# Optimization experiments

Hardware: AMD Instinct MI355X
Metric: run time of the kernel (lower is better)

The kernel has to match this reference:

```python
import jax, jax.numpy as jnp
import numpy as np

NUM_HEADS = 12
HEAD_DIM = 128
DIM = NUM_HEADS * HEAD_DIM  # 1536
FRAMES = 8
GRID_H, GRID_W = 15, 26
SPATIAL = GRID_H * GRID_W  # 390
SEQ = FRAMES * SPATIAL      # 3120
EPS = 1e-5


def setup_inputs() -> dict:
    key = jax.random.key(0)
    ks = jax.random.split(key, 12)
    w = lambda k, shape, s=0.02: jax.random.normal(k, shape, dtype=jnp.float32) * s
    return {
        "x": jax.random.normal(ks[0], (1, SEQ, DIM), dtype=jnp.float32),
        "freqs": jax.random.uniform(ks[1], (SEQ, HEAD_DIM // 2), dtype=jnp.float32) * 6.283,
        "Wq": w(ks[2], (DIM, DIM)), "bq": jnp.zeros((DIM,), jnp.float32), "gq": jnp.ones((DIM,), jnp.float32),
        "Wk": w(ks[3], (DIM, DIM)), "bk": jnp.zeros((DIM,), jnp.float32), "gk": jnp.ones((DIM,), jnp.float32),
        "Wv": w(ks[4], (DIM, DIM)), "bv": jnp.zeros((DIM,), jnp.float32),
        "Wo": w(ks[5], (DIM, DIM)), "bo": jnp.zeros((DIM,), jnp.float32),
        "qk_frame_bias": w(ks[6], (FRAMES, DIM), 0.05),
        "v_frame_bias": w(ks[7], (FRAMES, DIM), 0.05),
        "v_spatial_bias": w(ks[8], (SPATIAL, DIM), 0.05),
    }


def _rmsnorm(x, g):
    return x * jax.lax.rsqrt(jnp.mean(x * x, axis=-1, keepdims=True) + EPS) * g


def _rope(x, freqs):
    # x: [b, s, dim] -> per-head interleaved complex rotation (Wan-style)
    b, s, _ = x.shape
    xp = x.reshape(b, s, NUM_HEADS, HEAD_DIM // 2, 2)
    cos = jnp.cos(freqs)[None, :, None, :]  # [1, s, 1, d/2]
    sin = jnp.sin(freqs)[None, :, None, :]
    xr, xi = xp[..., 0], xp[..., 1]
    out = jnp.stack([xr * cos - xi * sin, xr * sin + xi * cos], axis=-1)
    return out.reshape(b, s, DIM)


def _expand_frame(bias):
    # [FRAMES, dim] -> [1, FRAMES*SPATIAL, dim] (each frame vector repeated over spatial tokens)
    return jnp.broadcast_to(bias[:, None, :], (FRAMES, SPATIAL, DIM)).reshape(1, SEQ, DIM)


def _expand_spatial(bias):
    # [SPATIAL, dim] -> [1, FRAMES*SPATIAL, dim] (tiled over frames)
    return jnp.broadcast_to(bias[None, :, :], (FRAMES, SPATIAL, DIM)).reshape(1, SEQ, DIM)


def reference(x, freqs, Wq, bq, gq, Wk, bk, gk, Wv, bv, Wo, bo,
              qk_frame_bias, v_frame_bias, v_spatial_bias):
    q = _rmsnorm(x @ Wq + bq, gq)
    k = _rmsnorm(x @ Wk + bk, gk)
    v = x @ Wv + bv
    q = _rope(q, freqs)
    k = _rope(k, freqs)
    qk_bias = _expand_frame(qk_frame_bias)
    q = q + qk_bias
    k = k + qk_bias
    v = v + _expand_frame(v_frame_bias) + _expand_spatial(v_spatial_bias)
    b, s, _ = x.shape
    qh = q.reshape(b, s, NUM_HEADS, HEAD_DIM)
    kh = k.reshape(b, s, NUM_HEADS, HEAD_DIM)
    vh = v.reshape(b, s, NUM_HEADS, HEAD_DIM)
    scale = 1.0 / np.sqrt(HEAD_DIM)
    scores = jnp.einsum("bqnd,bknd->bnqk", qh, kh) * scale
    attn = jax.nn.softmax(scores, axis=-1)
    out = jnp.einsum("bnqk,bknd->bqnd", attn, vh).reshape(b, s, DIM)
    return out @ Wo + bo
```

## Files before the change

### kernel.cpp

```cpp
#include <hip/hip_runtime.h>
#include <cstdint>

#define SEQ     3120
#define SPAD    3200
#define DIM     1536
#define NQKV    4608
#define HEADS   12
#define HD      128
#define SPATIAL 390
#define EPSV    1e-5f
#define KVBLK   64
#define NTILES  49
#define NEGBIG  (-1e30f)
#define QSCALE  (0.08838834764831845f * 1.4426950408889634f)
#define CROW(r, hi) ((((r) & 3) + 8 * ((r) >> 2)) + 4 * (hi))

typedef unsigned short u16;
typedef short s16x8 __attribute__((ext_vector_type(8)));
typedef float f32x4 __attribute__((ext_vector_type(4)));
typedef float f32x16 __attribute__((ext_vector_type(16)));

__device__ __forceinline__ u16 f2bf(float f) {
  union { float f; unsigned u; } v; v.f = f;
  unsigned r = v.u + 0x7FFFu + ((v.u >> 16) & 1u);
  return (u16)(r >> 16);
}
__device__ __forceinline__ float bf2f(u16 b) {
  union { unsigned u; float f; } v; v.u = ((unsigned)b) << 16;
  return v.f;
}
__device__ __forceinline__ unsigned cvtpk(float lo, float hi) {
  unsigned r;
  asm("v_cvt_pk_bf16_f32 %0, %1, %2" : "=v"(r) : "v"(lo), "v"(hi));
  return r;
}
__device__ __forceinline__ void gload16(const void* g, const void* l) {
  __builtin_amdgcn_global_load_lds(
      (const __attribute__((address_space(1))) unsigned*)g,
      (__attribute__((address_space(3))) unsigned*)(uintptr_t)l,
      16, 0, 0);
}

__global__ __launch_bounds__(256) void k_prep(
    const float* __restrict__ x, const float* __restrict__ bq,
    const float* __restrict__ bk, const float* __restrict__ bv,
    const float* __restrict__ Wq, const float* __restrict__ Wk,
    const float* __restrict__ Wv, const float* __restrict__ Wo,
    u16* __restrict__ xb, float* __restrict__ bcat,
    u16* __restrict__ WtAll, u16* __restrict__ WoT) {
  __shared__ float t[64][65];
  const int bid = blockIdx.x;
  if (bid < 4800) {
    if (bid == 0) {
      for (int j = threadIdx.x; j < NQKV; j += 256)
        bcat[j] = (j < DIM) ? bq[j] : (j < 2 * DIM) ? bk[j - DIM] : bv[j - 2 * DIM];
    }
    const int i = (bid * 256 + threadIdx.x) * 4;
    if (i >= SPAD * DIM) return;
    const int row = i / DIM;
    float4 v = make_float4(0.f, 0.f, 0.f, 0.f);
    if (row < SEQ) v = *(const float4*)(x + i);
    const unsigned lo = (unsigned)f2bf(v.x) | ((unsigned)f2bf(v.y) << 16);
    const unsigned hi = (unsigned)f2bf(v.z) | ((unsigned)f2bf(v.w) << 16);
    *(uint2*)(xb + i) = make_uint2(lo, hi);
  } else {
    const int tb = bid - 4800;
    const int wsel = tb / 576;
    const int rem = tb - wsel * 576;
    const int byi = rem / 24, bxi = rem - (rem / 24) * 24;
    const float* W = (wsel == 0) ? Wq : (wsel == 1) ? Wk : (wsel == 2) ? Wv : Wo;
    const int k0 = bxi * 64, n0 = byi * 64;
    const int c = threadIdx.x & 63, r4 = threadIdx.x >> 6;
#pragma unroll
    for (int rr = 0; rr < 64; rr += 4)
      t[r4 + rr][c] = W[(size_t)(k0 + r4 + rr) * DIM + n0 + c];
    __syncthreads();
    u16* Wt = (wsel < 3) ? (WtAll + (size_t)wsel * DIM * DIM) : WoT;
    const int kp = threadIdx.x & 31;
    const int r8 = threadIdx.x >> 5;
#pragma unroll
    for (int rr = 0; rr < 64; rr += 8) {
      const int n = r8 + rr;
      const unsigned v = (unsigned)f2bf(t[2 * kp][n]) |
                         ((unsigned)f2bf(t[2 * kp + 1][n]) << 16);
      *(unsigned*)&Wt[(size_t)(n0 + n) * DIM + k0 + 2 * kp] = v;
    }
  }
}

template <int OUT_BF16>
__global__ __launch_bounds__(256) void k_gemm(const u16* __restrict__ A,
                                              const u16* __restrict__ Bt,
                                              const float* __restrict__ bias,
                                              void* __restrict__ Cout,
                                              int N, int K, int storeMmax,
                                              int nbx) {
  __shared__ short As[2][8192];
  __shared__ short Bs[2][8192];
  const int nwg = gridDim.x;
  const int q = nwg >> 3, r = nwg & 7;
  const int xcd = blockIdx.x & 7, idx = blockIdx.x >> 3;
  const int swz = (xcd < r ? xcd * (q + 1) : r * (q + 1) + (xcd - r) * q) + idx;
  const int bxi = swz % nbx, byi = swz / nbx;
  const int brow = byi * 128, bcol = bxi * 128;

  const int tid = threadIdx.x;
  const int lane = tid & 63, wv = tid >> 6;
  const int l15 = lane & 15, g = lane >> 4;
  const int wr = wv >> 1, wc = wv & 1;

  const f32x4 z4 = {0.f, 0.f, 0.f, 0.f};
  f32x4 acc[4][4];
#pragma unroll
  for (int m = 0; m < 4; ++m)
#pragma unroll
    for (int n = 0; n < 4; ++n) acc[m][n] = z4;

  const u16* Ap[4];
  const u16* Bp[4];
  const int sch = ((lane & 7) ^ ((lane >> 3) & 7)) * 8;
#pragma unroll
  for (int it = 0; it < 4; ++it) {
    const int row = it * 32 + wv * 8 + (lane >> 3);
    Ap[it] = A + (size_t)(brow + row) * K + sch;
    Bp[it] = Bt + (size_t)(bcol + row) * K + sch;
  }
  auto stage = [&](int T, int B) {
    const int k0 = T * 64;
#pragma unroll
    for (int it = 0; it < 4; ++it) {
      gload16(Ap[it] + k0, &As[B][(it * 32 + wv * 8) * 64]);
      gload16(Bp[it] + k0, &Bs[B][(it * 32 + wv * 8) * 64]);
    }
  };

  const int NK = K >> 6;
  stage(0, 0);

  for (int t = 0; t < NK; ++t) {
    const int b = t & 1;
    if (t + 1 < NK) {
      stage(t + 1, b ^ 1);
      asm volatile("s_waitcnt vmcnt(8)" ::: "memory");
    } else {
      asm volatile("s_waitcnt vmcnt(0)" ::: "memory");
    }
    __builtin_amdgcn_s_barrier();
    __builtin_amdgcn_sched_barrier(0);
#pragma unroll
    for (int kk = 0; kk < 2; ++kk) {
      s16x8 a[4], bfr[4];
#pragma unroll
      for (int m = 0; m < 4; ++m)
        a[m] = *(const s16x8*)&As[b][(wr * 64 + m * 16 + l15) * 64 +
                                     (((kk * 4 + g) ^ (l15 & 7)) * 8)];
#pragma unroll
      for (int n = 0; n < 4; ++n)
        bfr[n] = *(const s16x8*)&Bs[b][(wc * 64 + n * 16 + l15) * 64 +
                                       (((kk * 4 + g) ^ (l15 & 7)) * 8)];
#pragma unroll
      for (int m = 0; m < 4; ++m)
#pragma unroll
        for (int n = 0; n < 4; ++n)
          acc[m][n] = __builtin_amdgcn_mfma_f32_16x16x32_bf16(a[m], bfr[n], acc[m][n], 0, 0, 0);
    }
    __builtin_amdgcn_s_barrier();
    __builtin_amdgcn_sched_barrier(0);
  }

#pragma unroll
  for (int m = 0; m < 4; ++m) {
#pragma unroll
    for (int n = 0; n < 4; ++n) {
      const int cc = bcol + wc * 64 + n * 16 + l15;
      const float bb = bias[cc];
#pragma unroll
      for (int i = 0; i < 4; ++i) {
        const int rr = brow + wr * 64 + m * 16 + g * 4 + i;
        if (rr < storeMmax) {
          const float v = acc[m][n][i] + bb;
          if (OUT_BF16) ((u16*)Cout)[(size_t)rr * N + cc] = f2bf(v);
          else          ((float*)Cout)[(size_t)rr * N + cc] = v;
        }
      }
    }
  }
}

__global__ __launch_bounds__(256) void k_post(
    const u16* __restrict__ Pqkv, const float* __restrict__ freqs,
    const float* __restrict__ gq, const float* __restrict__ gk,
    const float* __restrict__ qkfb, const float* __restrict__ vfb,
    const float* __restrict__ vsb,
    u16* __restrict__ Qf, u16* __restrict__ Kf, u16* __restrict__ Vf) {
  const int s = blockIdx.x;
  const int t = threadIdx.x;
  const int fidx = s / SPATIAL;
  const int sp = s - fidx * SPATIAL;
  __shared__ float cs[64], sn[64];
  __shared__ float red[8];
  if (t < 64) {
    const float a = freqs[s * 64 + t];
    cs[t] = __cosf(a);
    sn[t] = __sinf(a);
  }
  const u16* qrow = Pqkv + (size_t)s * NQKV;
  const u16* krow = qrow + DIM;
  const u16* vrow = qrow + 2 * DIM;
  s16x8 q8, k8, v8;
  float sq = 0.f, sk = 0.f;
  if (t < 192) {
    q8 = *(const s16x8*)(qrow + 8 * t);
    k8 = *(const s16x8*)(krow + 8 * t);
    v8 = *(const s16x8*)(vrow + 8 * t);
#pragma unroll
    for (int i = 0; i < 8; ++i) {
      const float a = bf2f((u16)q8[i]); sq += a * a;
      const float b = bf2f((u16)k8[i]); sk += b * b;
    }
  }
#pragma unroll
  for (int off = 1; off < 64; off <<= 1) {
    sq += __shfl_xor(sq, off);
    sk += __shfl_xor(sk, off);
  }
  const int lane = t & 63, wv = t >> 6;
  if (lane == 0) { red[wv] = sq; red[wv + 4] = sk; }
  __syncthreads();
  sq = red[0] + red[1] + red[2] + red[3];
  sk = red[4] + red[5] + red[6] + red[7];
  const float rq = rsqrtf(sq * (1.0f / DIM) + EPSV);
  const float rk = rsqrtf(sk * (1.0f / DIM) + EPSV);
  if (t >= 192) return;
  const int d0 = 8 * t;
  float GQ[8], GK[8], FB[8], VF[8], VS[8];
  *(float4*)&GQ[0] = *(const float4*)(gq + d0);
  *(float4*)&GQ[4] = *(const float4*)(gq + d0 + 4);
  *(float4*)&GK[0] = *(const float4*)(gk + d0);
  *(float4*)&GK[4] = *(const float4*)(gk + d0 + 4);
  *(float4*)&FB[0] = *(const float4*)(qkfb + fidx * DIM + d0);
  *(float4*)&FB[4] = *(const float4*)(qkfb + fidx * DIM + d0 + 4);
  *(float4*)&VF[0] = *(const float4*)(vfb + fidx * DIM + d0);
  *(float4*)&VF[4] = *(const float4*)(vfb + fidx * DIM + d0 + 4);
  *(float4*)&VS[0] = *(const float4*)(vsb + (size_t)sp * DIM + d0);
  *(float4*)&VS[4] = *(const float4*)(vsb + (size_t)sp * DIM + d0 + 4);
  unsigned qo[4], ko[4], vo[4];
#pragma unroll
  for (int pi = 0; pi < 4; ++pi) {
    const int pin = (4 * t + pi) & 63;
    const float c = cs[pin], s_ = sn[pin];
    float xr = bf2f((u16)q8[2 * pi]) * rq * GQ[2 * pi];
    float xi = bf2f((u16)q8[2 * pi + 1]) * rq * GQ[2 * pi + 1];
    const float q0 = (xr * c - xi * s_ + FB[2 * pi]) * QSCALE;
    const float q1 = (xr * s_ + xi * c + FB[2 * pi + 1]) * QSCALE;
    qo[pi] = (unsigned)f2bf(q0) | ((unsigned)f2bf(q1) << 16);
    xr = bf2f((u16)k8[2 * pi]) * rk * GK[2 * pi];
    xi = bf2f((u16)k8[2 * pi + 1]) * rk * GK[2 * pi + 1];
    const float kk0 = xr * c - xi * s_ + FB[2 * pi];
    const float kk1 = xr * s_ + xi * c + FB[2 * pi + 1];
    ko[pi] = (unsigned)f2bf(kk0) | ((unsigned)f2bf(kk1) << 16);
    const float v0 = bf2f((u16)v8[2 * pi]) + VF[2 * pi] + VS[2 * pi];
    const float v1 = bf2f((u16)v8[2 * pi + 1]) + VF[2 * pi + 1] + VS[2 * pi + 1];
    vo[pi] = (unsigned)f2bf(v0) | ((unsigned)f2bf(v1) << 16);
  }
  *(uint4*)(Qf + (size_t)s * DIM + d0) = make_uint4(qo[0], qo[1], qo[2], qo[3]);
  *(uint4*)(Kf + (size_t)s * DIM + d0) = make_uint4(ko[0], ko[1], ko[2], ko[3]);
  *(uint4*)(Vf + (size_t)s * DIM + d0) = make_uint4(vo[0], vo[1], vo[2], vo[3]);
}

__global__ __launch_bounds__(256) void k_transpose_v(const u16* __restrict__ Vf,
                                                     u16* __restrict__ Vt) {
  __shared__ u16 tile[64][65];
  const int s0 = blockIdx.x * 64, c0 = blockIdx.y * 64;
  const int c = threadIdx.x & 63, r4 = threadIdx.x >> 6;
#pragma unroll
  for (int rr = 0; rr < 64; rr += 4) {
    const int s = s0 + r4 + rr;
    tile[r4 + rr][c] = (s < SEQ) ? Vf[(size_t)s * DIM + c0 + c] : (u16)0;
  }
  __syncthreads();
#pragma unroll
  for (int rr = 0; rr < 64; rr += 4) {
    const int dglob = c0 + r4 + rr;
    Vt[(size_t)dglob * SPAD + s0 + c] = tile[c][r4 + rr];
  }
}

__global__ __launch_bounds__(320, 2) void k_attn(const u16* __restrict__ Qf,
                                                 const u16* __restrict__ Kf,
                                                 const u16* __restrict__ Vt,
                                                 u16* __restrict__ AttO) {
  __shared__ short Ks[2][8192];
  __shared__ short Vs[2][8192];
  const int bid = blockIdx.x;
  const int gb = (bid & 7) * 30 + (bid >> 3);
  const int h = gb / 20;
  const int bx = gb - h * 20;
  const int tid = threadIdx.x;
  const int lane = tid & 63, w = tid >> 6;
  const int l31 = lane & 31, hi = lane >> 5;
  const int qrow = bx * 160 + w * 32 + l31;

  s16x8 qb[8];
  {
    const u16* qp = Qf + (size_t)qrow * DIM + h * HD + hi * 8;
#pragma unroll
    for (int s = 0; s < 8; ++s) qb[s] = *(const s16x8*)(qp + s * 16);
  }

  f32x16 o[4];
#pragma unroll
  for (int d = 0; d < 4; ++d)
#pragma unroll
    for (int r = 0; r < 16; ++r) o[d][r] = 0.f;
  float sl = 0.f;

  const u16* Kp[4];
  const u16* Vp[4];
  if (w < 4) {
#pragma unroll
    for (int it = 0; it < 4; ++it) {
      const int krow = w * 16 + it * 4 + (lane >> 4);
      const int kch = (lane & 15) ^ (it * 4 + (lane >> 4));
      Kp[it] = Kf + (size_t)krow * DIM + h * HD + kch * 8;
      const int vrow = w * 32 + it * 8 + (lane >> 3);
      const int vch = (lane & 7) ^ (lane >> 3);
      Vp[it] = Vt + (size_t)(h * HD + vrow) * SPAD + vch * 8;
    }
  }
  auto stage = [&](int T, int B) {
    const size_t kof = (size_t)T * KVBLK * DIM;
    const int vof = T * KVBLK;
#pragma unroll
    for (int it = 0; it < 4; ++it) {
      gload16(Kp[it] + kof, &Ks[B][(w * 16 + it * 4) * 128]);
      gload16(Vp[it] + vof, &Vs[B][(w * 32 + it * 8) * 64]);
    }
  };

  if (w < 4) {
    asm volatile("s_waitcnt vmcnt(0)" ::: "memory");
    stage(0, 0);
  }

  for (int t = 0; t < NTILES; ++t) {
    const int b = t & 1;
    if (w < 4) {
      if (t + 1 < NTILES) {
        stage(t + 1, b ^ 1);
        asm volatile("s_waitcnt vmcnt(8)" ::: "memory");
      } else {
        asm volatile("s_waitcnt vmcnt(0)" ::: "memory");
      }
    }
    __builtin_amdgcn_s_barrier();
    __builtin_amdgcn_sched_barrier(0);

    f32x16 st[2];
#pragma unroll
    for (int r = 0; r < 16; ++r) { st[0][r] = 0.f; st[1][r] = 0.f; }
    __builtin_amdgcn_s_setprio(1);
#pragma unroll
    for (int grp = 0; grp < 2; ++grp)
#pragma unroll
      for (int s = 0; s < 8; ++s) {
        const s16x8 ka = *(const s16x8*)&Ks[b][(grp * 32 + l31) * 128 +
                                              (((2 * s + hi) ^ (lane & 15)) * 8)];
        st[grp] = __builtin_amdgcn_mfma_f32_32x32x16_bf16(ka, qb[s], st[grp], 0, 0, 0);
      }
    __builtin_amdgcn_s_setprio(0);

    s16x8 vb[4][4];
#pragma unroll
    for (int s = 0; s < 4; ++s)
#pragma unroll
      for (int d = 0; d < 4; ++d)
        vb[s][d] = *(const s16x8*)&Vs[b][(d * 32 + l31) * 64 +
                                         (((2 * s + hi) ^ (lane & 7)) * 8)];

    if (t == NTILES - 1) {
#pragma unroll
      for (int r = 8; r < 16; ++r) st[1][r] = NEGBIG;
    }
    unsigned W[16];
    float p0s = 0.f, p1s = 0.f, p2s = 0.f, p3s = 0.f;
#pragma unroll
    for (int grp = 0; grp < 2; ++grp)
#pragma unroll
      for (int i = 0; i < 8; ++i) {
        const float p0 = exp2f(st[grp][2 * i]);
        const float p1 = exp2f(st[grp][2 * i + 1]);
        if (grp) { p2s += p0; p3s += p1; } else { p0s += p0; p1s += p1; }
        W[grp * 8 + i] = cvtpk(p0, p1);
      }
    sl += (p0s + p1s) + (p2s + p3s);

    __builtin_amdgcn_s_setprio(1);
#pragma unroll
    for (int s = 0; s < 4; ++s) {
      const int base = (s >> 1) * 8 + (s & 1) * 4;
      unsigned a0 = W[base + 0], b0 = W[base + 2];
      unsigned a1 = W[base + 1], b1 = W[base + 3];
      asm volatile("v_permlane32_swap_b32 %0, %1" : "+v"(a0), "+v"(b0));
      asm volatile("v_permlane32_swap_b32 %0, %1" : "+v"(a1), "+v"(b1));
      unsigned pw[4] = {a0, a1, b0, b1};
      const s16x8 pa = *(const s16x8*)pw;
#pragma unroll
      for (int d = 0; d < 4; ++d)
        o[d] = __builtin_amdgcn_mfma_f32_32x32x16_bf16(pa, vb[s][d], o[d], 0, 0, 0);
    }
    __builtin_amdgcn_s_setprio(0);
    __builtin_amdgcn_s_barrier();
    __builtin_amdgcn_sched_barrier(0);
  }

  sl += __shfl_xor(sl, 32);
  const float rs = 1.0f / sl;
#pragma unroll
  for (int r = 0; r < 16; ++r) {
    const float rq = __shfl(rs, CROW(r, hi));
    const int row = bx * 160 + w * 32 + CROW(r, hi);
    if (row < SEQ) {
#pragma unroll
      for (int d = 0; d < 4; ++d)
        AttO[(size_t)row * DIM + h * HD + d * 32 + l31] = f2bf(o[d][r] * rq);
    }
  }
}

extern "C" void kernel_launch(void* const* d_in, const int* in_sizes, int n_in,
                              void* d_out, int out_size, void* d_ws, size_t ws_size,
                              hipStream_t stream) {
  const float* x    = (const float*)d_in[0];
  const float* freqs= (const float*)d_in[1];
  const float* Wq   = (const float*)d_in[2];
  const float* bq   = (const float*)d_in[3];
  const float* gq   = (const float*)d_in[4];
  const float* Wk   = (const float*)d_in[5];
  const float* bk   = (const float*)d_in[6];
  const float* gk   = (const float*)d_in[7];
  const float* Wv   = (const float*)d_in[8];
  const float* bv   = (const float*)d_in[9];
  const float* Wo   = (const float*)d_in[10];
  const float* bo   = (const float*)d_in[11];
  const float* qkfb = (const float*)d_in[12];
  const float* vfb  = (const float*)d_in[13];
  const float* vsb  = (const float*)d_in[14];

  if (ws_size < (size_t)87705600) return;

  char* ws = (char*)d_ws;
  u16*   xb    = (u16*)(ws);
  u16*   Vt    = (u16*)(ws);
  u16*   WtAll = (u16*)(ws + 9830400);
  u16*   WoT   = (u16*)(ws + 23986176);
  float* bcat  = (float*)(ws + 28704768);
  u16*   Pqkv  = (u16*)(ws + 28723200);
  u16*   AttO  = (u16*)(ws + 28723200);
  u16*   Qf    = (u16*)(ws + 58214400);
  u16*   Kf    = (u16*)(ws + 68044800);
  u16*   Vf    = (u16*)(ws + 77875200);

  k_prep<<<7104, 256, 0, stream>>>(x, bq, bk, bv, Wq, Wk, Wv, Wo,
                                   xb, bcat, WtAll, WoT);
  k_gemm<1><<<900, 256, 0, stream>>>(xb, WtAll, bcat, Pqkv, NQKV, DIM, SPAD, 36);
  k_post<<<SEQ, 256, 0, stream>>>(Pqkv, freqs, gq, gk, qkfb, vfb, vsb, Qf, Kf, Vf);
  k_transpose_v<<<dim3(50, 24), 256, 0, stream>>>(Vf, Vt);
  k_attn<<<240, 320, 0, stream>>>(Qf, Kf, Vt, AttO);
  k_gemm<0><<<300, 256, 0, stream>>>(AttO, WoT, bo, d_out, DIM, DIM, SEQ, 12);
}
```

Before: 236.9 us.

## Double attention KV tile to 128 and process score groups incrementally

Raises the K/V block staged into shared memory from 64 to 128 keys, halving the number of tile iterations and barriers. The score/softmax/PV work is restructured into four 32-key groups, each computing scores, exponentials and PV MFMAs in turn, with V fragments read from LDS per group instead of preloaded. The larger double buffers quadruple... doubling LDS usage, which likely reduces blocks per CU below the requested two, trading occupancy for fewer synchronizations.

```diff
diff --git a/kernel.cpp b/kernel.cpp
--- a/kernel.cpp
+++ b/kernel.cpp
@@ -9,8 +9,8 @@
 #define HD      128
 #define SPATIAL 390
 #define EPSV    1e-5f
-#define KVBLK   64
-#define NTILES  49
+#define KVBLK   128
+#define NTILES  25
 #define NEGBIG  (-1e30f)
 #define QSCALE  (0.08838834764831845f * 1.4426950408889634f)
 #define CROW(r, hi) ((((r) & 3) + 8 * ((r) >> 2)) + 4 * (hi))
@@ -290,8 +290,8 @@
                                                  const u16* __restrict__ Kf,
                                                  const u16* __restrict__ Vt,
                                                  u16* __restrict__ AttO) {
-  __shared__ short Ks[2][8192];
-  __shared__ short Vs[2][8192];
+  __shared__ short Ks[2][16384];
+  __shared__ short Vs[2][16384];
   const int bid = blockIdx.x;
   const int gb = (bid & 7) * 30 + (bid >> 3);
   const int h = gb / 20;
@@ -315,16 +315,16 @@
     for (int r = 0; r < 16; ++r) o[d][r] = 0.f;
   float sl = 0.f;
 
-  const u16* Kp[4];
-  const u16* Vp[4];
+  const u16* Kp[8];
+  const u16* Vp[8];
   if (w < 4) {
 #pragma unroll
-    for (int it = 0; it < 4; ++it) {
-      const int krow = w * 16 + it * 4 + (lane >> 4);
-      const int kch = (lane & 15) ^ (it * 4 + (lane >> 4));
+    for (int it = 0; it < 8; ++it) {
+      const int krow = w * 32 + it * 4 + (lane >> 4);
+      const int kch = (lane & 15) ^ (krow & 15);
       Kp[it] = Kf + (size_t)krow * DIM + h * HD + kch * 8;
-      const int vrow = w * 32 + it * 8 + (lane >> 3);
-      const int vch = (lane & 7) ^ (lane >> 3);
+      const int vrow = w * 32 + it * 4 + (lane >> 4);
+      const int vch = (lane & 15) ^ (vrow & 15);
       Vp[it] = Vt + (size_t)(h * HD + vrow) * SPAD + vch * 8;
     }
   }
@@ -332,9 +332,9 @@
     const size_t kof = (size_t)T * KVBLK * DIM;
     const int vof = T * KVBLK;
 #pragma unroll
-    for (int it = 0; it < 4; ++it) {
-      gload16(Kp[it] + kof, &Ks[B][(w * 16 + it * 4) * 128]);
-      gload16(Vp[it] + vof, &Vs[B][(w * 32 + it * 8) * 64]);
+    for (int it = 0; it < 8; ++it) {
+      gload16(Kp[it] + kof, &Ks[B][(w * 32 + it * 4) * 128]);
+      gload16(Vp[it] + vof, &Vs[B][(w * 32 + it * 4) * 128]);
     }
   };
 
@@ -348,7 +348,7 @@
     if (w < 4) {
       if (t + 1 < NTILES) {
         stage(t + 1, b ^ 1);
-        asm volatile("s_waitcnt vmcnt(8)" ::: "memory");
+        asm volatile("s_waitcnt vmcnt(16)" ::: "memory");
       } else {
         asm volatile("s_waitcnt vmcnt(0)" ::: "memory");
       }
@@ -356,60 +356,59 @@
     __builtin_amdgcn_s_barrier();
     __builtin_amdgcn_sched_barrier(0);
 
-    f32x16 st[2];
-#pragma unroll
-    for (int r = 0; r < 16; ++r) { st[0][r] = 0.f; st[1][r] = 0.f; }
-    __builtin_amdgcn_s_setprio(1);
-#pragma unroll
-    for (int grp = 0; grp < 2; ++grp)
+#pragma unroll
+    for (int grp = 0; grp < 4; ++grp) {
+      f32x16 st;
+#pragma unroll
+      for (int r = 0; r < 16; ++r) st[r] = 0.f;
+      __builtin_amdgcn_s_setprio(1);
 #pragma unroll
       for (int s = 0; s < 8; ++s) {
         const s16x8 ka = *(const s16x8*)&Ks[b][(grp * 32 + l31) * 128 +
                                               (((2 * s + hi) ^ (lane & 15)) * 8)];
-        st[grp] = __builtin_amdgcn_mfma_f32_32x32x16_bf16(ka, qb[s], st[grp], 0, 0, 0);
-      }
-    __builtin_amdgcn_s_setprio(0);
-
-    s16x8 vb[4][4];
-#pragma unroll
-    for (int s = 0; s < 4; ++s)
-#pragma unroll
-      for (int d = 0; d < 4; ++d)
-        vb[s][d] = *(const s16x8*)&Vs[b][(d * 32 + l31) * 64 +
-                                         (((2 * s + hi) ^ (lane & 7)) * 8)];
-
-    if (t == NTILES - 1) {
-#pragma unroll
-      for (int r = 8; r < 16; ++r) st[1][r] = NEGBIG;
-    }
-    unsigned W[16];
-    float p0s = 0.f, p1s = 0.f, p2s = 0.f, p3s = 0.f;
-#pragma unroll
-    for (int grp = 0; grp < 2; ++grp)
+        st = __builtin_amdgcn_mfma_f32_32x32x16_bf16(ka, qb[s], st, 0, 0, 0);
+      }
+      __builtin_amdgcn_s_setprio(0);
+
+      if (t == NTILES - 1) {
+        if (grp == 1) {
+#pragma unroll
+          for (int r = 8; r < 16; ++r) st[r] = NEGBIG;
+        } else if (grp >= 2) {
+#pragma unroll
+          for (int r = 0; r < 16; ++r) st[r] = NEGBIG;
+        }
+      }
+      unsigned W[8];
+      float p0s = 0.f, p1s = 0.f;
 #pragma unroll
       for (int i = 0; i < 8; ++i) {
-        const float p0 = exp2f(st[grp][2 * i]);
-        const float p1 = exp2f(st[grp][2 * i + 1]);
-        if (grp) { p2s += p0; p3s += p1; } else { p0s += p0; p1s += p1; }
-        W[grp * 8 + i] = cvtpk(p0, p1);
-      }
-    sl += (p0s + p1s) + (p2s + p3s);
-
-    __builtin_amdgcn_s_setprio(1);
-#pragma unroll
-    for (int s = 0; s < 4; ++s) {
-      const int base = (s >> 1) * 8 + (s & 1) * 4;
-      unsigned a0 = W[base + 0], b0 = W[base + 2];
-      unsigned a1 = W[base + 1], b1 = W[base + 3];
-      asm volatile("v_permlane32_swap_b32 %0, %1" : "+v"(a0), "+v"(b0));
-      asm volatile("v_permlane32_swap_b32 %0, %1" : "+v"(a1), "+v"(b1));
-      unsigned pw[4] = {a0, a1, b0, b1};
-      const s16x8 pa = *(const s16x8*)pw;
-#pragma unroll
-      for (int d = 0; d < 4; ++d)
-        o[d] = __builtin_amdgcn_mfma_f32_32x32x16_bf16(pa, vb[s][d], o[d], 0, 0, 0);
-    }
-    __builtin_amdgcn_s_setprio(0);
+        const float p0 = exp2f(st[2 * i]);
+        const float p1 = exp2f(st[2 * i + 1]);
+        p0s += p0; p1s += p1;
+        W[i] = cvtpk(p0, p1);
+      }
+      sl += p0s + p1s;
+
+      __builtin_amdgcn_s_setprio(1);
+#pragma unroll
+      for (int s2 = 0; s2 < 2; ++s2) {
+        const int S = grp * 2 + s2;
+        unsigned a0 = W[s2 * 4 + 0], b0 = W[s2 * 4 + 2];
+        unsigned a1 = W[s2 * 4 + 1], b1 = W[s2 * 4 + 3];
+        asm volatile("v_permlane32_swap_b32 %0, %1" : "+v"(a0), "+v"(b0));
+        asm volatile("v_permlane32_swap_b32 %0, %1" : "+v"(a1), "+v"(b1));
+        unsigned pw[4] = {a0, a1, b0, b1};
+        const s16x8 pa = *(const s16x8*)pw;
+#pragma unroll
+        for (int d = 0; d < 4; ++d) {
+          const s16x8 vbf = *(const s16x8*)&Vs[b][(d * 32 + l31) * 128 +
+                                                 (((2 * S + hi) ^ (lane & 15)) * 8)];
+          o[d] = __builtin_amdgcn_mfma_f32_32x32x16_bf16(pa, vbf, o[d], 0, 0, 0);
+        }
+      }
+      __builtin_amdgcn_s_setprio(0);
+    }
     __builtin_amdgcn_s_barrier();
     __builtin_amdgcn_sched_barrier(0);
   }
```

Measured after the change: 232.4 us (median of 2 runs). About the same (-1.9%).
